# Performance work log

Measured on AMD Instinct MI355X. Metric: run time of the kernel, lower is better.

The kernel has to match this reference:

```python
import jax, jax.numpy as jnp
import numpy as np

NEG_INF = -9e15  # matches the -9000000000000000.0 mask constant in the torch code
ALPHA = 0.2      # LeakyReLU negative slope


def setup_inputs() -> dict:
    key = jax.random.key(0)
    ks = jax.random.split(key, 8)
    N, F = 8192, 256
    h = jax.random.normal(ks[0], (N, F), dtype=jnp.float32)
    adj = jax.random.randint(ks[1], (N, N), 0, 2).astype(jnp.float32)
    W = jax.random.normal(ks[2], (F, F), dtype=jnp.float32) * 0.05
    a = jax.random.normal(ks[3], (2 * F, 1), dtype=jnp.float32) * 0.05
    w_ih = jax.random.normal(ks[4], (3 * F, F), dtype=jnp.float32) * 0.05
    w_hh = jax.random.normal(ks[5], (3 * F, F), dtype=jnp.float32) * 0.05
    b_ih = jax.random.normal(ks[6], (3 * F,), dtype=jnp.float32) * 0.05
    b_hh = jax.random.normal(ks[7], (3 * F,), dtype=jnp.float32) * 0.05
    return {"h": h, "adj": adj, "W": W, "a": a,
            "w_ih": w_ih, "w_hh": w_hh, "b_ih": b_ih, "b_hh": b_hh}


def reference(h, adj, W, a, w_ih, w_hh, b_ih, b_hh):
    F_out = W.shape[1]
    Wh = h @ W  # [N, F]
    # a_input @ a decomposes exactly: e_ij = leakyrelu(Wh_i . a[:F] + Wh_j . a[F:])
    src = Wh @ a[:F_out]   # [N, 1]
    dst = Wh @ a[F_out:]   # [N, 1]
    e = jax.nn.leaky_relu(src + dst.T, ALPHA)          # [N, N]
    att = jnp.where(adj > 0, e, NEG_INF)
    att = jax.nn.softmax(att, axis=1)                   # dropout: eval mode (identity)
    h_prime = att @ Wh                                  # [N, F]
    # torch GRUCell(h_prime, h)
    gi = h_prime @ w_ih.T + b_ih                        # [N, 3F]
    gh = h @ w_hh.T + b_hh
    i_r, i_z, i_n = jnp.split(gi, 3, axis=1)
    h_r, h_z, h_n = jnp.split(gh, 3, axis=1)
    r = jax.nn.sigmoid(i_r + h_r)
    z = jax.nn.sigmoid(i_z + h_z)
    n = jnp.tanh(i_n + r * h_n)
    return (1.0 - z) * n + z * h
```

## Files before the change

### kernel.cpp

```cpp
#include <hip/hip_runtime.h>

typedef __attribute__((ext_vector_type(8))) short bf16x8;
typedef __attribute__((ext_vector_type(4))) float f32x4;
typedef unsigned short u16;
typedef unsigned int u32;

#define NN 8192
#define FD 256

__device__ __forceinline__ u16 f2bf(float f) {
  union { float f; unsigned u; } v; v.f = f;
  unsigned r = v.u + 0x7FFF + ((v.u >> 16) & 1);
  return (u16)(r >> 16);
}

__device__ __forceinline__ bf16x8 ldcvt8(const float* __restrict__ p) {
  f32x4 x0 = *(const f32x4*)p;
  f32x4 x1 = *(const f32x4*)(p + 4);
  bf16x8 t;
  t[0] = (short)f2bf(x0[0]); t[1] = (short)f2bf(x0[1]);
  t[2] = (short)f2bf(x0[2]); t[3] = (short)f2bf(x0[3]);
  t[4] = (short)f2bf(x1[0]); t[5] = (short)f2bf(x1[1]);
  t[6] = (short)f2bf(x1[2]); t[7] = (short)f2bf(x1[3]);
  return t;
}

__device__ __forceinline__ void gl16(const void* g, void* l) {
  __builtin_amdgcn_global_load_lds((const __attribute__((address_space(1))) u32*)g,
                                   (__attribute__((address_space(3))) u32*)l, 16, 0, 0);
}

__global__ __launch_bounds__(256) void k_zero(float* __restrict__ p) {
  size_t g = (size_t)(blockIdx.x * 256 + threadIdx.x) * 4;
  f32x4 z = {0.f, 0.f, 0.f, 0.f};
  *(f32x4*)(p + g) = z;
}

__global__ __launch_bounds__(256) void k_wh(const float* __restrict__ h,
                                            const float* __restrict__ W,
                                            const float* __restrict__ a,
                                            u16* __restrict__ whT,
                                            float* __restrict__ src,
                                            float* __restrict__ dst) {
  int tid = threadIdx.x;
  int lane = tid & 63;
  int wv = tid >> 6;
  int r0 = blockIdx.x * 64 + (wv >> 1) * 32;
  int c0 = blockIdx.y * 64 + (wv & 1) * 32;
  int lr = lane & 15;
  int q = lane >> 4;

  f32x4 acc[2][2] = {};
  for (int kk = 0; kk < FD; kk += 32) {
    int kb = kk + q * 8;
    bf16x8 av[2], bv[2];
#pragma unroll
    for (int m = 0; m < 2; m++)
      av[m] = ldcvt8(h + (size_t)(r0 + m * 16 + lr) * FD + kb);
#pragma unroll
    for (int n = 0; n < 2; n++) {
      int col = c0 + n * 16 + lr;
      const float* p = W + (size_t)kb * FD + col;
      bf16x8 t;
#pragma unroll
      for (int e = 0; e < 8; e++) t[e] = (short)f2bf(p[(size_t)e * FD]);
      bv[n] = t;
    }
#pragma unroll
    for (int m = 0; m < 2; m++)
#pragma unroll
      for (int n = 0; n < 2; n++)
        acc[m][n] = __builtin_amdgcn_mfma_f32_16x16x32_bf16(av[m], bv[n], acc[m][n], 0, 0, 0);
  }
#pragma unroll
  for (int m = 0; m < 2; m++)
#pragma unroll
    for (int n = 0; n < 2; n++) {
      int gc = c0 + n * 16 + lr;
      int gr = r0 + m * 16 + q * 4;
      ushort4 st;
      st.x = f2bf(acc[m][n][0]);
      st.y = f2bf(acc[m][n][1]);
      st.z = f2bf(acc[m][n][2]);
      st.w = f2bf(acc[m][n][3]);
      *(ushort4*)(whT + (size_t)gc * NN + gr) = st;
    }
  float aA0 = a[c0 + lr], aA1 = a[c0 + 16 + lr];
  float aB0 = a[256 + c0 + lr], aB1 = a[256 + c0 + 16 + lr];
#pragma unroll
  for (int m = 0; m < 2; m++)
#pragma unroll
    for (int j = 0; j < 4; j++) {
      float s1 = acc[m][0][j] * aA0 + acc[m][1][j] * aA1;
      float s2 = acc[m][0][j] * aB0 + acc[m][1][j] * aB1;
#pragma unroll
      for (int sh = 1; sh < 16; sh <<= 1) {
        s1 += __shfl_xor(s1, sh);
        s2 += __shfl_xor(s2, sh);
      }
      if (lr == 0) {
        int row = r0 + m * 16 + q * 4 + j;
        atomicAdd(&src[row], s1);
        atomicAdd(&dst[row], s2);
      }
    }
}

__global__ __launch_bounds__(512, 4) void k_att(const float* __restrict__ adj,
                                                const u16* __restrict__ whT,
                                                const float* __restrict__ src,
                                                const float* __restrict__ dst,
                                                float* __restrict__ hp,
                                                float* __restrict__ lg) {
  __shared__ u16 wbuf[4][8192];
  __shared__ float dst_lds[2048];

  const int tid = threadIdx.x;
  const int lane = tid & 63;
  const int w = tid >> 6;
  const int lr = lane & 15;
  const int q = lane >> 4;
  const int rg = w >> 1;
  const int ch = w & 1;
  const int bid = blockIdx.x;
  const int jh = bid & 3;
  const int i0 = (bid >> 2) * 64;
  const int jb = jh * 2048;

  const float* adjP = adj + (size_t)(i0 + rg * 16 + lr) * NN + jb + q * 8;
  const float srcv = src[i0 + rg * 16 + lr];

  const int gc = w * 32 + (lane >> 2);
  const int jslot = (lane & 3) ^ ((lane >> 3) & 3);
  const u16* wsrc0 = whT + (size_t)gc * NN + jb + jslot * 8;
  const u16* wsrc1 = wsrc0 + (size_t)16 * NN;

  const int dsb = (ch * 128 + lr) * 32 + (q ^ ((lr >> 1) & 3)) * 8;

  f32x4 acc[8] = {};
  float lsum = 0.f;
  f32x4 aA0, aA1, aB0, aB1;
  bf16x8 AF;

#define G(T)                                                                \
  {                                                                         \
    gl16(wsrc0 + (size_t)(T) * 32, &wbuf[(T) & 3][w * 1024]);               \
    gl16(wsrc1 + (size_t)(T) * 32, &wbuf[(T) & 3][w * 1024 + 512]);         \
  }
#define ALOAD(T, R0, R1)                                                    \
  {                                                                         \
    R0 = *(const f32x4*)(adjP + (size_t)(T) * 32);                          \
    R1 = *(const f32x4*)(adjP + (size_t)(T) * 32 + 4);                      \
  }
#define ACOMP(T, R0, R1)                                                    \
  {                                                                         \
    f32x4 d0 = *(const f32x4*)&dst_lds[(T) * 32 + q * 8];                   \
    f32x4 d1 = *(const f32x4*)&dst_lds[(T) * 32 + q * 8 + 4];               \
    _Pragma("unroll") for (int e = 0; e < 4; e++) {                         \
      float x = srcv + d0[e];                                               \
      x = fmaxf(x, 0.2f * x);                                               \
      float p = R0[e] * __expf(x);                                          \
      lsum += p;                                                            \
      AF[e] = (short)f2bf(p);                                               \
    }                                                                       \
    _Pragma("unroll") for (int e = 0; e < 4; e++) {                         \
      float x = srcv + d1[e];                                               \
      x = fmaxf(x, 0.2f * x);                                               \
      float p = R1[e] * __expf(x);                                          \
      lsum += p;                                                            \
      AF[4 + e] = (short)f2bf(p);                                           \
    }                                                                       \
  }
#define CMPS(T)                                                             \
  {                                                                         \
    const u16* pb = &wbuf[(T) & 3][0];                                      \
    _Pragma("unroll") for (int bn = 0; bn < 8; bn++) {                      \
      bf16x8 bf = *(const bf16x8*)&pb[dsb + bn * 512];                      \
      acc[bn] = __builtin_amdgcn_mfma_f32_16x16x32_bf16(AF, bf, acc[bn], 0, 0, 0); \
    }                                                                       \
  }
#define LBARV asm volatile("s_waitcnt vmcnt(6) lgkmcnt(0)\n\ts_barrier" ::: "memory")

  *(f32x4*)&dst_lds[tid * 4] = *(const f32x4*)(dst + jb + tid * 4);
  G(0);
  G(1);
  ALOAD(0, aA0, aA1);
  ALOAD(1, aB0, aB1);
  __syncthreads();

  for (int t = 0; t < 64; t += 2) {
    if (t + 2 < 64) G(t + 2);
    ACOMP(t, aA0, aA1);
    if (t + 2 < 64) ALOAD(t + 2, aA0, aA1);
    LBARV;
    CMPS(t);
    if (t + 3 < 64) G(t + 3);
    ACOMP(t + 1, aB0, aB1);
    if (t + 3 < 64) ALOAD(t + 3, aB0, aB1);
    LBARV;
    CMPS(t + 1);
  }
#undef G
#undef ALOAD
#undef ACOMP
#undef CMPS
#undef LBARV

  lsum += __shfl_xor(lsum, 16);
  lsum += __shfl_xor(lsum, 32);
  if (ch == 0 && q == 0) atomicAdd(&lg[i0 + rg * 16 + lr], lsum);

#pragma unroll
  for (int bn = 0; bn < 8; bn++)
#pragma unroll
    for (int j = 0; j < 4; j++)
      atomicAdd(&hp[(size_t)(i0 + rg * 16 + q * 4 + j) * FD + ch * 128 + bn * 16 + lr],
                acc[bn][j]);
}

__global__ __launch_bounds__(256) void k_norm(const float* __restrict__ hp,
                                              const float* __restrict__ lg,
                                              u16* __restrict__ hpb) {
  int g = blockIdx.x * 1024 + threadIdx.x * 4;
  f32x4 v = *(const f32x4*)(hp + g);
  float inv = 1.0f / lg[g >> 8];
  ushort4 st;
  st.x = f2bf(v[0] * inv);
  st.y = f2bf(v[1] * inv);
  st.z = f2bf(v[2] * inv);
  st.w = f2bf(v[3] * inv);
  *(ushort4*)(hpb + g) = st;
}

__global__ __launch_bounds__(256) void k_gru(const u16* __restrict__ hpb,
                                             const float* __restrict__ h,
                                             const float* __restrict__ wih,
                                             const float* __restrict__ whh,
                                             const float* __restrict__ bih,
                                             const float* __restrict__ bhh,
                                             float* __restrict__ out) {
  int tid = threadIdx.x;
  int lane = tid & 63;
  int wv = tid >> 6;
  int i0 = blockIdx.x * 32;
  int lr = lane & 15;
  int q = lane >> 4;
  int c = blockIdx.y * 64 + wv * 16 + lr;
  f32x4 gi[3][2] = {};
  f32x4 gh[3][2] = {};
  for (int kk = 0; kk < FD; kk += 32) {
    int kb = kk + q * 8;
    bf16x8 ap[2], ah[2], bi[3], bh[3];
#pragma unroll
    for (int m = 0; m < 2; m++) {
      ap[m] = *(const bf16x8*)(hpb + (size_t)(i0 + m * 16 + lr) * FD + kb);
      ah[m] = ldcvt8(h + (size_t)(i0 + m * 16 + lr) * FD + kb);
    }
#pragma unroll
    for (int g = 0; g < 3; g++) {
      bi[g] = ldcvt8(wih + (size_t)(g * 256 + c) * FD + kb);
      bh[g] = ldcvt8(whh + (size_t)(g * 256 + c) * FD + kb);
    }
#pragma unroll
    for (int g = 0; g < 3; g++)
#pragma unroll
      for (int m = 0; m < 2; m++) {
        gi[g][m] = __builtin_amdgcn_mfma_f32_16x16x32_bf16(ap[m], bi[g], gi[g][m], 0, 0, 0);
        gh[g][m] = __builtin_amdgcn_mfma_f32_16x16x32_bf16(ah[m], bh[g], gh[g][m], 0, 0, 0);
      }
  }
  float bir = bih[c], biz = bih[256 + c], bin = bih[512 + c];
  float bhr = bhh[c], bhz = bhh[256 + c], bhn = bhh[512 + c];
#pragma unroll
  for (int m = 0; m < 2; m++)
#pragma unroll
    for (int j = 0; j < 4; j++) {
      int row = i0 + m * 16 + q * 4 + j;
      float rv = gi[0][m][j] + bir + gh[0][m][j] + bhr;
      float zv = gi[1][m][j] + biz + gh[1][m][j] + bhz;
      float r = 1.f / (1.f + __expf(-rv));
      float z = 1.f / (1.f + __expf(-zv));
      float nx = gi[2][m][j] + bin + r * (gh[2][m][j] + bhn);
      float n = 1.f - 2.f / (__expf(2.f * nx) + 1.f);
      float hv = h[(size_t)row * FD + c];
      out[(size_t)row * FD + c] = (1.f - z) * n + z * hv;
    }
}

extern "C" void kernel_launch(void* const* d_in, const int* in_sizes, int n_in,
                              void* d_out, int out_size, void* d_ws, size_t ws_size,
                              hipStream_t stream) {
  const float* h   = (const float*)d_in[0];
  const float* adj = (const float*)d_in[1];
  const float* W   = (const float*)d_in[2];
  const float* a   = (const float*)d_in[3];
  const float* wih = (const float*)d_in[4];
  const float* whh = (const float*)d_in[5];
  const float* bih = (const float*)d_in[6];
  const float* bhh = (const float*)d_in[7];
  float* out = (float*)d_out;

  char* ws = (char*)d_ws;
  u16* whT   = (u16*)(ws);
  u16* hpb   = (u16*)(ws);
  float* hp  = (float*)(ws + 4194304);
  float* lg  = (float*)(ws + 12582912);
  float* srcv = (float*)(ws + 12615680);
  float* dstv = (float*)(ws + 12648448);
  (void)ws_size;

  k_zero<<<2072, 256, 0, stream>>>((float*)(ws + 4194304));
  k_wh<<<dim3(128, 4), 256, 0, stream>>>(h, W, a, whT, srcv, dstv);
  k_att<<<512, 512, 0, stream>>>(adj, whT, srcv, dstv, hp, lg);
  k_norm<<<2048, 256, 0, stream>>>(hp, lg, hpb);
  k_gru<<<dim3(256, 4), 256, 0, stream>>>(hpb, h, wih, whh, bih, bhh, out);
}
```

Baseline: 229.9 us.

## Restructure attention GEMM: stage probabilities in LDS, load WhT fragments directly

New measurement: 284.2 us. 23.6% more time.

```diff
diff --git a/kernel.cpp b/kernel.cpp
--- a/kernel.cpp
+++ b/kernel.cpp
@@ -23,11 +23,6 @@
   t[4] = (short)f2bf(x1[0]); t[5] = (short)f2bf(x1[1]);
   t[6] = (short)f2bf(x1[2]); t[7] = (short)f2bf(x1[3]);
   return t;
-}
-
-__device__ __forceinline__ void gl16(const void* g, void* l) {
-  __builtin_amdgcn_global_load_lds((const __attribute__((address_space(1))) u32*)g,
-                                   (__attribute__((address_space(3))) u32*)l, 16, 0, 0);
 }
 
 __global__ __launch_bounds__(256) void k_zero(float* __restrict__ p) {
@@ -106,13 +101,13 @@
     }
 }
 
-__global__ __launch_bounds__(512, 4) void k_att(const float* __restrict__ adj,
+__global__ __launch_bounds__(512, 2) void k_att(const float* __restrict__ adj,
                                                 const u16* __restrict__ whT,
                                                 const float* __restrict__ src,
                                                 const float* __restrict__ dst,
                                                 float* __restrict__ hp,
                                                 float* __restrict__ lg) {
-  __shared__ u16 wbuf[4][8192];
+  __shared__ u16 pbuf[3][4096];
   __shared__ float dst_lds[2048];
 
   const int tid = threadIdx.x;
@@ -120,102 +115,107 @@
   const int w = tid >> 6;
   const int lr = lane & 15;
   const int q = lane >> 4;
-  const int rg = w >> 1;
-  const int ch = w & 1;
   const int bid = blockIdx.x;
   const int jh = bid & 3;
-  const int i0 = (bid >> 2) * 64;
+  const int i0 = (bid >> 2) * 128;
   const int jb = jh * 2048;
 
-  const float* adjP = adj + (size_t)(i0 + rg * 16 + lr) * NN + jb + q * 8;
-  const float srcv = src[i0 + rg * 16 + lr];
-
-  const int gc = w * 32 + (lane >> 2);
-  const int jslot = (lane & 3) ^ ((lane >> 3) & 3);
-  const u16* wsrc0 = whT + (size_t)gc * NN + jb + jslot * 8;
-  const u16* wsrc1 = wsrc0 + (size_t)16 * NN;
-
-  const int dsb = (ch * 128 + lr) * 32 + (q ^ ((lr >> 1) & 3)) * 8;
-
-  f32x4 acc[8] = {};
+  const int pr = tid >> 2;
+  const int jq = tid & 3;
+  const float* adjP = adj + (size_t)(i0 + pr) * NN + jb + jq * 8;
+  const float srcv = src[i0 + pr];
+  const int pwo = pr * 32 + ((jq ^ (pr & 3)) * 8);
+
+  const int c0 = w * 32;
+  const u16* wp = whT + (size_t)(c0 + lr) * NN + jb + q * 8;
+  const int bro = lr * 32 + ((q ^ (lr & 3)) * 8);
+
+  f32x4 acc[2][8] = {};
   float lsum = 0.f;
-  f32x4 aA0, aA1, aB0, aB1;
-  bf16x8 AF;
-
-#define G(T)                                                                \
+  f32x4 a0a, a0b, a1a, a1b;
+  bf16x8 A0[2], A1[2];
+
+  *(f32x4*)&dst_lds[tid * 4] = *(const f32x4*)(dst + jb + tid * 4);
+
+#define ALD(T, X, Y)                                                        \
+  { X = *(const f32x4*)(adjP + (size_t)(T) * 32);                           \
+    Y = *(const f32x4*)(adjP + (size_t)(T) * 32 + 4); }
+#define AF(T, A)                                                            \
+  { A[0] = *(const bf16x8*)(wp + (size_t)(T) * 32);                         \
+    A[1] = *(const bf16x8*)(wp + (size_t)16 * NN + (T) * 32); }
+#define PGEN(T, X, Y, B)                                                    \
   {                                                                         \
-    gl16(wsrc0 + (size_t)(T) * 32, &wbuf[(T) & 3][w * 1024]);               \
-    gl16(wsrc1 + (size_t)(T) * 32, &wbuf[(T) & 3][w * 1024 + 512]);         \
-  }
-#define ALOAD(T, R0, R1)                                                    \
-  {                                                                         \
-    R0 = *(const f32x4*)(adjP + (size_t)(T) * 32);                          \
-    R1 = *(const f32x4*)(adjP + (size_t)(T) * 32 + 4);                      \
-  }
-#define ACOMP(T, R0, R1)                                                    \
-  {                                                                         \
-    f32x4 d0 = *(const f32x4*)&dst_lds[(T) * 32 + q * 8];                   \
-    f32x4 d1 = *(const f32x4*)&dst_lds[(T) * 32 + q * 8 + 4];               \
+    bf16x8 s;                                                               \
     _Pragma("unroll") for (int e = 0; e < 4; e++) {                         \
-      float x = srcv + d0[e];                                               \
+      float x = srcv + dst_lds[(T) * 32 + jq * 8 + e];                      \
       x = fmaxf(x, 0.2f * x);                                               \
-      float p = R0[e] * __expf(x);                                          \
+      float p = X[e] * __expf(x);                                           \
       lsum += p;                                                            \
-      AF[e] = (short)f2bf(p);                                               \
+      s[e] = (short)f2bf(p);                                                \
     }                                                                       \
     _Pragma("unroll") for (int e = 0; e < 4; e++) {                         \
-      float x = srcv + d1[e];                                               \
+      float x = srcv + dst_lds[(T) * 32 + jq * 8 + 4 + e];                  \
       x = fmaxf(x, 0.2f * x);                                               \
-      float p = R1[e] * __expf(x);                                          \
+      float p = Y[e] * __expf(x);                                           \
       lsum += p;                                                            \
-      AF[4 + e] = (short)f2bf(p);                                           \
+      s[4 + e] = (short)f2bf(p);                                            \
     }                                                                       \
-  }
-#define CMPS(T)                                                             \
+    *(bf16x8*)&pbuf[B][pwo] = s;                                            \
+  }
+#define CMP(A, B)                                                           \
   {                                                                         \
-    const u16* pb = &wbuf[(T) & 3][0];                                      \
-    _Pragma("unroll") for (int bn = 0; bn < 8; bn++) {                      \
-      bf16x8 bf = *(const bf16x8*)&pb[dsb + bn * 512];                      \
-      acc[bn] = __builtin_amdgcn_mfma_f32_16x16x32_bf16(AF, bf, acc[bn], 0, 0, 0); \
+    _Pragma("unroll") for (int nb = 0; nb < 8; nb++) {                      \
+      bf16x8 bf = *(const bf16x8*)&pbuf[B][nb * 512 + bro];                 \
+      acc[0][nb] = __builtin_amdgcn_mfma_f32_16x16x32_bf16(A[0], bf, acc[0][nb], 0, 0, 0); \
+      acc[1][nb] = __builtin_amdgcn_mfma_f32_16x16x32_bf16(A[1], bf, acc[1][nb], 0, 0, 0); \
     }                                                                       \
   }
-#define LBARV asm volatile("s_waitcnt vmcnt(6) lgkmcnt(0)\n\ts_barrier" ::: "memory")
-
-  *(f32x4*)&dst_lds[tid * 4] = *(const f32x4*)(dst + jb + tid * 4);
-  G(0);
-  G(1);
-  ALOAD(0, aA0, aA1);
-  ALOAD(1, aB0, aB1);
+#define LBAR asm volatile("s_waitcnt lgkmcnt(0)\n\ts_barrier" ::: "memory")
+
+  ALD(0, a0a, a0b);
+  ALD(1, a1a, a1b);
+  AF(0, A0);
   __syncthreads();
-
+  PGEN(0, a0a, a0b, 0);
+  LBAR;
+
+  int r = 0;
   for (int t = 0; t < 64; t += 2) {
-    if (t + 2 < 64) G(t + 2);
-    ACOMP(t, aA0, aA1);
-    if (t + 2 < 64) ALOAD(t + 2, aA0, aA1);
-    LBARV;
-    CMPS(t);
-    if (t + 3 < 64) G(t + 3);
-    ACOMP(t + 1, aB0, aB1);
-    if (t + 3 < 64) ALOAD(t + 3, aB0, aB1);
-    LBARV;
-    CMPS(t + 1);
-  }
-#undef G
-#undef ALOAD
-#undef ACOMP
-#undef CMPS
-#undef LBARV
-
-  lsum += __shfl_xor(lsum, 16);
-  lsum += __shfl_xor(lsum, 32);
-  if (ch == 0 && q == 0) atomicAdd(&lg[i0 + rg * 16 + lr], lsum);
-
-#pragma unroll
-  for (int bn = 0; bn < 8; bn++)
-#pragma unroll
-    for (int j = 0; j < 4; j++)
-      atomicAdd(&hp[(size_t)(i0 + rg * 16 + q * 4 + j) * FD + ch * 128 + bn * 16 + lr],
-                acc[bn][j]);
+    int wr = (r == 2) ? 0 : r + 1;
+    if (t + 2 < 64) ALD(t + 2, a0a, a0b);
+    AF(t + 1, A1);
+    PGEN(t + 1, a1a, a1b, wr);
+    CMP(A0, r);
+    LBAR;
+    r = wr;
+    wr = (r == 2) ? 0 : r + 1;
+    if (t + 3 < 64) ALD(t + 3, a1a, a1b);
+    if (t + 2 < 64) {
+      AF(t + 2, A0);
+      PGEN(t + 2, a0a, a0b, wr);
+    }
+    CMP(A1, r);
+    LBAR;
+    r = wr;
+  }
+#undef ALD
+#undef AF
+#undef PGEN
+#undef CMP
+#undef LBAR
+
+  lsum += __shfl_xor(lsum, 1);
+  lsum += __shfl_xor(lsum, 2);
+  if (jq == 0) atomicAdd(&lg[i0 + pr], lsum);
+
+#pragma unroll
+  for (int na = 0; na < 2; na++)
+#pragma unroll
+    for (int nb = 0; nb < 8; nb++)
+#pragma unroll
+      for (int j = 0; j < 4; j++)
+        atomicAdd(&hp[(size_t)(i0 + nb * 16 + lr) * FD + c0 + na * 16 + q * 4 + j],
+                  acc[na][nb][j]);
 }
 
 __global__ __launch_bounds__(256) void k_norm(const float* __restrict__ hp,
@@ -311,7 +311,7 @@
 
   k_zero<<<2072, 256, 0, stream>>>((float*)(ws + 4194304));
   k_wh<<<dim3(128, 4), 256, 0, stream>>>(h, W, a, whT, srcv, dstv);
-  k_att<<<512, 512, 0, stream>>>(adj, whT, srcv, dstv, hp, lg);
+  k_att<<<256, 512, 0, stream>>>(adj, whT, srcv, dstv, hp, lg);
   k_norm<<<2048, 256, 0, stream>>>(hp, lg, hpb);
   k_gru<<<dim3(256, 4), 256, 0, stream>>>(hpb, h, wih, whh, bih, bhh, out);
 }
```

## Load attention B operand directly into registers instead of LDS staging

Applied to the files above, without the earlier changes.

New measurement: 413.8 us. +80.0%, slower.

```diff
diff --git a/kernel.cpp b/kernel.cpp
--- a/kernel.cpp
+++ b/kernel.cpp
@@ -23,11 +23,6 @@
   t[4] = (short)f2bf(x1[0]); t[5] = (short)f2bf(x1[1]);
   t[6] = (short)f2bf(x1[2]); t[7] = (short)f2bf(x1[3]);
   return t;
-}
-
-__device__ __forceinline__ void gl16(const void* g, void* l) {
-  __builtin_amdgcn_global_load_lds((const __attribute__((address_space(1))) u32*)g,
-                                   (__attribute__((address_space(3))) u32*)l, 16, 0, 0);
 }
 
 __global__ __launch_bounds__(256) void k_zero(float* __restrict__ p) {
@@ -106,13 +101,12 @@
     }
 }
 
-__global__ __launch_bounds__(512, 4) void k_att(const float* __restrict__ adj,
+__global__ __launch_bounds__(256, 3) void k_att(const float* __restrict__ adj,
                                                 const u16* __restrict__ whT,
                                                 const float* __restrict__ src,
                                                 const float* __restrict__ dst,
                                                 float* __restrict__ hp,
                                                 float* __restrict__ lg) {
-  __shared__ u16 wbuf[4][8192];
   __shared__ float dst_lds[2048];
 
   const int tid = threadIdx.x;
@@ -120,102 +114,87 @@
   const int w = tid >> 6;
   const int lr = lane & 15;
   const int q = lane >> 4;
-  const int rg = w >> 1;
-  const int ch = w & 1;
   const int bid = blockIdx.x;
   const int jh = bid & 3;
-  const int i0 = (bid >> 2) * 64;
   const int jb = jh * 2048;
-
-  const float* adjP = adj + (size_t)(i0 + rg * 16 + lr) * NN + jb + q * 8;
-  const float srcv = src[i0 + rg * 16 + lr];
-
-  const int gc = w * 32 + (lane >> 2);
-  const int jslot = (lane & 3) ^ ((lane >> 3) & 3);
-  const u16* wsrc0 = whT + (size_t)gc * NN + jb + jslot * 8;
-  const u16* wsrc1 = wsrc0 + (size_t)16 * NN;
-
-  const int dsb = (ch * 128 + lr) * 32 + (q ^ ((lr >> 1) & 3)) * 8;
+  const int i0r = (bid >> 2) * 32 + (w >> 1) * 16;
+  const int c0 = (w & 1) * 128;
+
+  const float* adjP = adj + (size_t)(i0r + lr) * NN + jb + q * 8;
+  const float srcv = src[i0r + lr];
+  const u16* wp = whT + (size_t)(c0 + lr) * NN + jb + q * 8;
+
+  {
+    f32x4 v0 = *(const f32x4*)(dst + jb + tid * 8);
+    f32x4 v1 = *(const f32x4*)(dst + jb + tid * 8 + 4);
+    *(f32x4*)&dst_lds[tid * 8] = v0;
+    *(f32x4*)&dst_lds[tid * 8 + 4] = v1;
+  }
+  __syncthreads();
 
   f32x4 acc[8] = {};
   float lsum = 0.f;
   f32x4 aA0, aA1, aB0, aB1;
+  bf16x8 BfA[8], BfB[8];
   bf16x8 AF;
 
-#define G(T)                                                                \
-  {                                                                         \
-    gl16(wsrc0 + (size_t)(T) * 32, &wbuf[(T) & 3][w * 1024]);               \
-    gl16(wsrc1 + (size_t)(T) * 32, &wbuf[(T) & 3][w * 1024 + 512]);         \
-  }
-#define ALOAD(T, R0, R1)                                                    \
-  {                                                                         \
-    R0 = *(const f32x4*)(adjP + (size_t)(T) * 32);                          \
-    R1 = *(const f32x4*)(adjP + (size_t)(T) * 32 + 4);                      \
-  }
-#define ACOMP(T, R0, R1)                                                    \
+#define ALD(T, X, Y)                                                        \
+  { X = *(const f32x4*)(adjP + (size_t)(T) * 32);                           \
+    Y = *(const f32x4*)(adjP + (size_t)(T) * 32 + 4); }
+#define BLD(T, B)                                                           \
+  { _Pragma("unroll") for (int cf = 0; cf < 8; cf++)                        \
+      B[cf] = *(const bf16x8*)(wp + (size_t)cf * 16 * NN + (T) * 32); }
+#define PGEN(T, X, Y)                                                       \
   {                                                                         \
     f32x4 d0 = *(const f32x4*)&dst_lds[(T) * 32 + q * 8];                   \
     f32x4 d1 = *(const f32x4*)&dst_lds[(T) * 32 + q * 8 + 4];               \
     _Pragma("unroll") for (int e = 0; e < 4; e++) {                         \
       float x = srcv + d0[e];                                               \
       x = fmaxf(x, 0.2f * x);                                               \
-      float p = R0[e] * __expf(x);                                          \
+      float p = X[e] * __expf(x);                                           \
       lsum += p;                                                            \
       AF[e] = (short)f2bf(p);                                               \
     }                                                                       \
     _Pragma("unroll") for (int e = 0; e < 4; e++) {                         \
       float x = srcv + d1[e];                                               \
       x = fmaxf(x, 0.2f * x);                                               \
-      float p = R1[e] * __expf(x);                                          \
+      float p = Y[e] * __expf(x);                                           \
       lsum += p;                                                            \
       AF[4 + e] = (short)f2bf(p);                                           \
     }                                                                       \
   }
-#define CMPS(T)                                                             \
-  {                                                                         \
-    const u16* pb = &wbuf[(T) & 3][0];                                      \
-    _Pragma("unroll") for (int bn = 0; bn < 8; bn++) {                      \
-      bf16x8 bf = *(const bf16x8*)&pb[dsb + bn * 512];                      \
-      acc[bn] = __builtin_amdgcn_mfma_f32_16x16x32_bf16(AF, bf, acc[bn], 0, 0, 0); \
-    }                                                                       \
-  }
-#define LBARV asm volatile("s_waitcnt vmcnt(6) lgkmcnt(0)\n\ts_barrier" ::: "memory")
-
-  *(f32x4*)&dst_lds[tid * 4] = *(const f32x4*)(dst + jb + tid * 4);
-  G(0);
-  G(1);
-  ALOAD(0, aA0, aA1);
-  ALOAD(1, aB0, aB1);
-  __syncthreads();
+#define CMP(B)                                                              \
+  { _Pragma("unroll") for (int cf = 0; cf < 8; cf++)                        \
+      acc[cf] = __builtin_amdgcn_mfma_f32_16x16x32_bf16(AF, B[cf], acc[cf], 0, 0, 0); }
+
+  ALD(0, aA0, aA1);
+  BLD(0, BfA);
+  ALD(1, aB0, aB1);
+  BLD(1, BfB);
 
   for (int t = 0; t < 64; t += 2) {
-    if (t + 2 < 64) G(t + 2);
-    ACOMP(t, aA0, aA1);
-    if (t + 2 < 64) ALOAD(t + 2, aA0, aA1);
-    LBARV;
-    CMPS(t);
-    if (t + 3 < 64) G(t + 3);
-    ACOMP(t + 1, aB0, aB1);
-    if (t + 3 < 64) ALOAD(t + 3, aB0, aB1);
-    LBARV;
-    CMPS(t + 1);
-  }
-#undef G
-#undef ALOAD
-#undef ACOMP
-#undef CMPS
-#undef LBARV
+    PGEN(t, aA0, aA1);
+    CMP(BfA);
+    if (t + 2 < 64) { ALD(t + 2, aA0, aA1); BLD(t + 2, BfA); }
+    PGEN(t + 1, aB0, aB1);
+    CMP(BfB);
+    if (t + 3 < 64) { ALD(t + 3, aB0, aB1); BLD(t + 3, BfB); }
+  }
+#undef ALD
+#undef BLD
+#undef PGEN
+#undef CMP
 
   lsum += __shfl_xor(lsum, 16);
   lsum += __shfl_xor(lsum, 32);
-  if (ch == 0 && q == 0) atomicAdd(&lg[i0 + rg * 16 + lr], lsum);
-
-#pragma unroll
-  for (int bn = 0; bn < 8; bn++)
+  if ((w & 1) == 0 && lane < 16) atomicAdd(&lg[i0r + lane], lsum);
+
+#pragma unroll
+  for (int cf = 0; cf < 8; cf++)
 #pragma unroll
     for (int j = 0; j < 4; j++)
-      atomicAdd(&hp[(size_t)(i0 + rg * 16 + q * 4 + j) * FD + ch * 128 + bn * 16 + lr],
-                acc[bn][j]);
+      atomicAdd(&hp[(size_t)(i0r + q * 4 + j) * FD + c0 + cf * 16 + lr],
+                acc[cf][j]);
 }
 
 __global__ __launch_bounds__(256) void k_norm(const float* __restrict__ hp,
@@ -311,7 +290,7 @@
 
   k_zero<<<2072, 256, 0, stream>>>((float*)(ws + 4194304));
   k_wh<<<dim3(128, 4), 256, 0, stream>>>(h, W, a, whT, srcv, dstv);
-  k_att<<<512, 512, 0, stream>>>(adj, whT, srcv, dstv, hp, lg);
+  k_att<<<1024, 256, 0, stream>>>(adj, whT, srcv, dstv, hp, lg);
   k_norm<<<2048, 256, 0, stream>>>(hp, lg, hpb);
   k_gru<<<dim3(256, 4), 256, 0, stream>>>(hpb, h, wih, whh, bih, bhh, out);
 }
```
